# Kernel tuning notes

Measured on AMD Instinct MI355X. Metric: run time of the kernel, lower is better.

## Reference

```python
import jax, jax.numpy as jnp
import numpy as np

D_MODEL = 768
N_HEADS = 8
HEAD_DIM = D_MODEL // N_HEADS  # 96


def setup_inputs() -> dict:
    key = jax.random.key(0)
    k1, k2, k3, k4, k5 = jax.random.split(key, 5)
    B, LQ, LK = 2, 4096, 4096
    hidden_states = jax.random.normal(k1, (B, LQ, D_MODEL), dtype=jnp.float32)
    key_value_states = jax.random.normal(k2, (B, LK, D_MODEL), dtype=jnp.float32)
    # learned projection params (initialized as eye in torch, but learned; use random here)
    Wq = jax.random.normal(k3, (D_MODEL, D_MODEL), dtype=jnp.float32) * 0.02
    Wk = jax.random.normal(k4, (D_MODEL, D_MODEL), dtype=jnp.float32) * 0.02
    Wv = jax.random.normal(k5, (D_MODEL, D_MODEL), dtype=jnp.float32) * 0.02
    return {"hidden_states": hidden_states, "key_value_states": key_value_states,
            "Wq": Wq, "Wk": Wk, "Wv": Wv}


def reference(hidden_states, key_value_states, Wq, Wk, Wv):
    B, LQ, _ = hidden_states.shape
    LK = key_value_states.shape[1]
    # linear projections (no bias)
    q = hidden_states @ Wq            # [B, LQ, D]
    k = key_value_states @ Wk         # [B, LK, D]
    v = key_value_states @ Wv         # [B, LK, D]
    # split heads: [B, H, L, d]
    def shape(x, L):
        return x.reshape(B, L, N_HEADS, HEAD_DIM).transpose(0, 2, 1, 3)
    q = shape(q, LQ) / jnp.sqrt(jnp.float32(HEAD_DIM))
    k = shape(k, LK)
    v = shape(v, LK)
    scores = jnp.einsum('bhqd,bhkd->bhqk', q, k)   # [B, H, LQ, LK]
    attn = jax.nn.softmax(scores, axis=-1)
    # dropout p=0.0 -> identity
    ctx = jnp.einsum('bhqk,bhkd->bhqd', attn, v)   # [B, H, LQ, d]
    context = ctx.transpose(0, 2, 1, 3).reshape(B, LQ, D_MODEL)
    return context
```

## Files before the change

kernel.cpp:

```cpp
#include <hip/hip_runtime.h>
#include <hip/hip_bf16.h>


typedef __bf16 bf16x8 __attribute__((ext_vector_type(8)));
typedef __bf16 bf16x4 __attribute__((ext_vector_type(4)));
typedef float  f32x4  __attribute__((ext_vector_type(4)));
typedef float  f32x16 __attribute__((ext_vector_type(16)));
typedef unsigned u32x4 __attribute__((ext_vector_type(4)));

#define DM   768
#define NH   8
#define HD   96
#define SEQ  4096
#define BATCH 2
#define WELEM (DM*DM)
#define XELEM (BATCH*SEQ*DM)

#define GLDS16(gp, lp) __builtin_amdgcn_global_load_lds( \
    (const __attribute__((address_space(1))) void*)(gp), \
    (__attribute__((address_space(3))) void*)(lp), 16, 0, 0)

__global__ __launch_bounds__(256) void transpose_w3(
    const float* __restrict__ Wq, const float* __restrict__ Wk, const float* __restrict__ Wv,
    __bf16* __restrict__ Tq, __bf16* __restrict__ Tk, __bf16* __restrict__ Tv)
{
    int tid = blockIdx.x * 256 + threadIdx.x;
    int which = tid / WELEM;
    int e = tid - which * WELEM;
    int k = e / DM, n = e - k * DM;
    const float* W = (which == 0) ? Wq : (which == 1) ? Wk : Wv;
    __bf16* T      = (which == 0) ? Tq : (which == 1) ? Tk : Tv;
    T[n * DM + k] = (__bf16)W[e];
}

__global__ __launch_bounds__(256) void convert_x(
    const float* __restrict__ X0, const float* __restrict__ X1,
    __bf16* __restrict__ Y0, __bf16* __restrict__ Y1)
{
    const float* X = blockIdx.y ? X1 : X0;
    __bf16* Y      = blockIdx.y ? Y1 : Y0;
    const size_t i = ((size_t)blockIdx.x * 256 + threadIdx.x) * 8;
    float4 lo = *reinterpret_cast<const float4*>(X + i);
    float4 hi = *reinterpret_cast<const float4*>(X + i + 4);
    bf16x8 v;
    v[0]=(__bf16)lo.x; v[1]=(__bf16)lo.y; v[2]=(__bf16)lo.z; v[3]=(__bf16)lo.w;
    v[4]=(__bf16)hi.x; v[5]=(__bf16)hi.y; v[6]=(__bf16)hi.z; v[7]=(__bf16)hi.w;
    *reinterpret_cast<bf16x8*>(Y + i) = v;
}

__global__ __launch_bounds__(256, 2) void proj_gemm128(
    const __bf16* __restrict__ Xb, const __bf16* __restrict__ Wt,
    __bf16* __restrict__ Y, int mode, float scale)
{
    __shared__ __bf16 As[2][128][64];
    __shared__ __bf16 Bs[2][128][64];

    const int t = threadIdx.x;
    const int l = t & 63;
    const int w = t >> 6;
    const int ln = l & 15, g = l >> 4;
    const int wm = w >> 1, wn = w & 1;

    const int id = blockIdx.x;
    const int xcd = id & 7, c = id >> 3;
    const int m0 = (xcd * 8 + c / 6) * 128;
    const int n0 = (c % 6) * 128;

    size_t asrc[4], bsrc[4]; unsigned sdst[4];
    #pragma unroll
    for (int j = 0; j < 4; ++j) {
        const int cid = j * 256 + t;
        const int r = cid >> 3, cc = cid & 7, cs = cc ^ (r & 7);
        asrc[j] = (size_t)(m0 + r) * DM + cs * 8;
        bsrc[j] = (size_t)(n0 + r) * DM + cs * 8;
        sdst[j] = cid * 16;
    }

    f32x4 acc[4][4] = {};

    #pragma unroll
    for (int j = 0; j < 4; ++j) GLDS16(Xb + asrc[j], (char*)As + sdst[j]);
    #pragma unroll
    for (int j = 0; j < 4; ++j) GLDS16(Wt + bsrc[j], (char*)Bs + sdst[j]);
    __syncthreads();

    const int NKT = DM / 64;
    for (int kt = 0; kt < NKT; ++kt) {
        const int cur = kt & 1;
        if (kt + 1 < NKT) {
            const unsigned nb = (cur ^ 1) * 16384u;
            const size_t k0n = (size_t)(kt + 1) * 64;
            #pragma unroll
            for (int j = 0; j < 4; ++j) GLDS16(Xb + k0n + asrc[j], (char*)As + nb + sdst[j]);
            #pragma unroll
            for (int j = 0; j < 4; ++j) GLDS16(Wt + k0n + bsrc[j], (char*)Bs + nb + sdst[j]);
        }

        #pragma unroll
        for (int kk = 0; kk < 2; ++kk) {
            bf16x8 a[4], b[4];
            #pragma unroll
            for (int ms = 0; ms < 4; ++ms) {
                const int row = wm * 64 + ms * 16 + ln;
                const int slot = (kk * 4 + g) ^ (row & 7);
                a[ms] = *reinterpret_cast<const bf16x8*>(
                    (const char*)As + cur * 16384 + row * 128 + slot * 16);
            }
            #pragma unroll
            for (int ns = 0; ns < 4; ++ns) {
                const int row = wn * 64 + ns * 16 + ln;
                const int slot = (kk * 4 + g) ^ (row & 7);
                b[ns] = *reinterpret_cast<const bf16x8*>(
                    (const char*)Bs + cur * 16384 + row * 128 + slot * 16);
            }
            #pragma unroll
            for (int ms = 0; ms < 4; ++ms)
                #pragma unroll
                for (int ns = 0; ns < 4; ++ns)
                    acc[ms][ns] = __builtin_amdgcn_mfma_f32_16x16x32_bf16(
                        a[ms], b[ns], acc[ms][ns], 0, 0, 0);
        }
        __syncthreads();
    }

    #pragma unroll
    for (int ms = 0; ms < 4; ++ms) {
        #pragma unroll
        for (int ns = 0; ns < 4; ++ns) {
            const int col = n0 + wn * 64 + ns * 16 + ln;
            const int h = col / HD, d = col - h * HD;
            const int row_base = m0 + wm * 64 + ms * 16 + 4 * g;
            if (mode == 0) {
                #pragma unroll
                for (int r = 0; r < 4; ++r) {
                    const int row = row_base + r;
                    const int b_ = row >> 12, q = row & (SEQ - 1);
                    Y[(((size_t)(b_ * NH + h) * SEQ) + q) * HD + d] =
                        (__bf16)(acc[ms][ns][r] * scale);
                }
            } else {
                const int b_ = row_base >> 12, kq = row_base & (SEQ - 1);
                bf16x4 v;
                #pragma unroll
                for (int r = 0; r < 4; ++r) v[r] = (__bf16)acc[ms][ns][r];
                *reinterpret_cast<bf16x4*>(
                    &Y[((size_t)(b_ * NH + h) * HD + d) * SEQ + kq]) = v;
            }
        }
    }
}

__global__ __launch_bounds__(256, 2) void attn_kernel(
    const __bf16* __restrict__ Q, const __bf16* __restrict__ K,
    const __bf16* __restrict__ Vt, float* __restrict__ out)
{
    __shared__ __bf16 Ks[2][64][128];
    __shared__ __bf16 Vs[2][96][64];

    const int t = threadIdx.x;
    const int l = t & 63;
    const int w = t >> 6;
    const int lh = l >> 5;
    const int c31 = l & 31;

    const int swz = (blockIdx.x & 7) * 64 + (blockIdx.x >> 3);
    const int bh = swz >> 5;
    const int qb = swz & 31;
    const int b = bh >> 3, hd = bh & 7;
    const int q0 = qb * 128 + w * 32;

    const size_t base = (size_t)bh * SEQ * HD;
    const __bf16* Kg = K + base;
    const __bf16* Vg = Vt + base;

    size_t ksrc[4], vsrc[3];
    unsigned kdst[4], vdst[3];
    #pragma unroll
    for (int j = 0; j < 4; ++j) {
        const int cid = (w * 4 + j) * 64 + l;
        const int r = cid >> 4, cc = cid & 15;
        int cs = cc ^ (r & 7); if (cs >= 12) cs = 0;
        ksrc[j] = (size_t)r * HD + cs * 8;
        kdst[j] = (w * 4 + j) * 1024;
    }
    #pragma unroll
    for (int j = 0; j < 3; ++j) {
        const int cid = (w * 3 + j) * 64 + l;
        const int d = cid >> 3, cc = cid & 7;
        const int cs = cc ^ (d & 7);
        vsrc[j] = (size_t)d * SEQ + cs * 8;
        vdst[j] = (w * 3 + j) * 1024;
    }

    bf16x8 qb_[6];
    #pragma unroll
    for (int st = 0; st < 6; ++st)
        qb_[st] = *reinterpret_cast<const bf16x8*>(
            &Q[base + (size_t)(q0 + c31) * HD + st * 16 + 8 * lh]);

    f32x16 acc[3] = {};
    float m_r = -1e30f, l_r = 0.f;

    #pragma unroll
    for (int j = 0; j < 4; ++j) GLDS16(Kg + ksrc[j], (char*)Ks + kdst[j]);
    #pragma unroll
    for (int j = 0; j < 3; ++j) GLDS16(Vg + vsrc[j], (char*)Vs + vdst[j]);
    __syncthreads();

    const int NT = SEQ / 64;
    for (int kt = 0; kt < NT; ++kt) {
        const int cur = kt & 1;

        if (kt + 1 < NT) {
            const unsigned nb = (cur ^ 1);
            #pragma unroll
            for (int j = 0; j < 4; ++j)
                GLDS16(Kg + (size_t)(kt + 1) * 64 * HD + ksrc[j],
                       (char*)Ks + nb * 16384 + kdst[j]);
            #pragma unroll
            for (int j = 0; j < 3; ++j)
                GLDS16(Vg + (size_t)(kt + 1) * 64 + vsrc[j],
                       (char*)Vs + nb * 12288 + vdst[j]);
        }

        f32x16 s[2] = {};
        __builtin_amdgcn_s_setprio(1);
        #pragma unroll
        for (int ks = 0; ks < 2; ++ks) {
            const int rr = ks * 32 + c31;
            #pragma unroll
            for (int st = 0; st < 6; ++st) {
                const int slot = (2 * st + lh) ^ (rr & 7);
                bf16x8 ka = *reinterpret_cast<const bf16x8*>(
                    (const char*)Ks + cur * 16384 + rr * 256 + slot * 16);
                s[ks] = __builtin_amdgcn_mfma_f32_32x32x16_bf16(ka, qb_[st], s[ks], 0, 0, 0);
            }
        }
        __builtin_amdgcn_s_setprio(0);

        float tm = s[0][0];
        #pragma unroll
        for (int ks = 0; ks < 2; ++ks)
            #pragma unroll
            for (int r = 0; r < 16; ++r) tm = fmaxf(tm, s[ks][r]);
        {
            float ex = tm;
            asm volatile("" : "+v"(ex));
            asm("v_permlane32_swap_b32 %0, %1" : "+v"(ex), "+v"(tm));
            tm = fmaxf(tm, ex);
        }
        if (__any(tm > m_r + 8.f)) {
            const float mn = fmaxf(m_r, tm);
            const float al = __builtin_amdgcn_exp2f(m_r - mn);
            l_r *= al; m_r = mn;
            #pragma unroll
            for (int r = 0; r < 16; ++r) {
                const float ar = __shfl(al, (r & 3) + 8 * (r >> 2) + 4 * lh, 64);
                acc[0][r] *= ar; acc[1][r] *= ar; acc[2][r] *= ar;
            }
        }
        float ps = 0.f;
        #pragma unroll
        for (int ks = 0; ks < 2; ++ks)
            #pragma unroll
            for (int r = 0; r < 16; ++r) {
                const float p = __builtin_amdgcn_exp2f(s[ks][r] - m_r);
                s[ks][r] = p;
                ps += p;
            }
        {
            float ex = ps;
            asm volatile("" : "+v"(ex));
            asm("v_permlane32_swap_b32 %0, %1" : "+v"(ex), "+v"(ps));
            ps += ex;
        }
        l_r += ps;

        unsigned up[2][4][2];
        #pragma unroll
        for (int ks = 0; ks < 2; ++ks)
            #pragma unroll
            for (int qd = 0; qd < 4; ++qd)
                #pragma unroll
                for (int j = 0; j < 2; ++j)
                    asm("v_cvt_pk_bf16_f32 %0, %1, %2"
                        : "=v"(up[ks][qd][j])
                        : "v"(s[ks][4 * qd + 2 * j]), "v"(s[ks][4 * qd + 2 * j + 1]));

        #pragma unroll
        for (int kc = 0; kc < 4; ++kc) {
            const int ks = kc >> 1, cp = kc & 1;
            unsigned x0 = up[ks][2 * cp][0],     x1 = up[ks][2 * cp][1];
            unsigned y0 = up[ks][2 * cp + 1][0], y1 = up[ks][2 * cp + 1][1];
            asm("v_permlane32_swap_b32 %0, %1" : "+v"(x0), "+v"(y0));
            asm("v_permlane32_swap_b32 %0, %1" : "+v"(x1), "+v"(y1));
            u32x4 pw; pw[0] = x0; pw[1] = x1; pw[2] = y0; pw[3] = y1;
            const bf16x8 pa = __builtin_bit_cast(bf16x8, pw);
            __builtin_amdgcn_s_setprio(1);
            #pragma unroll
            for (int dt = 0; dt < 3; ++dt) {
                const int dd = dt * 32 + c31;
                const int slot = (2 * kc + lh) ^ (dd & 7);
                bf16x8 vb = *reinterpret_cast<const bf16x8*>(
                    (const char*)Vs + cur * 12288 + dd * 128 + slot * 16);
                acc[dt] = __builtin_amdgcn_mfma_f32_32x32x16_bf16(pa, vb, acc[dt], 0, 0, 0);
            }
            __builtin_amdgcn_s_setprio(0);
        }

        __syncthreads();
    }

    const float inv = 1.0f / l_r;
    #pragma unroll
    for (int r = 0; r < 16; ++r) {
        const int ql = (r & 3) + 8 * (r >> 2) + 4 * lh;
        const float ir = __shfl(inv, ql, 64);
        const int q = q0 + ql;
        float* dst = out + ((size_t)(b * SEQ + q)) * DM + hd * HD;
        #pragma unroll
        for (int dt = 0; dt < 3; ++dt)
            dst[dt * 32 + c31] = acc[dt][r] * ir;
    }
}

extern "C" void kernel_launch(void* const* d_in, const int* in_sizes, int n_in,
                              void* d_out, int out_size, void* d_ws, size_t ws_size,
                              hipStream_t stream) {
    const float* hidden = (const float*)d_in[0];
    const float* kv     = (const float*)d_in[1];
    const float* Wq     = (const float*)d_in[2];
    const float* Wk     = (const float*)d_in[3];
    const float* Wv     = (const float*)d_in[4];
    float* out = (float*)d_out;

    __bf16* Wt_q = (__bf16*)d_ws;
    __bf16* Wt_k = Wt_q + WELEM;
    __bf16* Wt_v = Wt_k + WELEM;
    __bf16* Qb   = Wt_v + WELEM;
    __bf16* Kb   = Qb + (size_t)BATCH * NH * SEQ * HD;
    __bf16* Vtb  = Kb + (size_t)BATCH * NH * SEQ * HD;

    __bf16* Xh_bf  = (__bf16*)d_out;
    __bf16* Xkv_bf = Xh_bf + XELEM;

    transpose_w3<<<3 * (WELEM / 256), 256, 0, stream>>>(Wq, Wk, Wv, Wt_q, Wt_k, Wt_v);
    convert_x<<<dim3(XELEM / 8 / 256, 2), 256, 0, stream>>>(hidden, kv, Xh_bf, Xkv_bf);

    const float qscale = 0.10206207261596575f * 1.4426950408889634f;
    proj_gemm128<<<384, 256, 0, stream>>>(Xh_bf,  Wt_q, Qb,  0, qscale);
    proj_gemm128<<<384, 256, 0, stream>>>(Xkv_bf, Wt_k, Kb,  0, 1.0f);
    proj_gemm128<<<384, 256, 0, stream>>>(Xkv_bf, Wt_v, Vtb, 1, 1.0f);

    attn_kernel<<<512, 256, 0, stream>>>(Qb, Kb, Vtb, out);
}
```

Measured before the change: 209.2 us.

## Process two 32-row query tiles per wave in attention kernel

Each wave now handles 64 query rows (two 32-row sub-tiles), so a block covers 256 queries and the grid drops from 512 to 256 blocks. Every K and V fragment read from LDS feeds two MFMAs, which halves LDS and global K/V traffic per query. The cost is more registers per thread, so launch bounds fall to one block per SIMD group. With only 256 blocks on a 256-CU device there is one wave per SIMD, leaving little latency hiding and no tail balancing.

```diff
diff --git a/kernel.cpp b/kernel.cpp
--- a/kernel.cpp
+++ b/kernel.cpp
@@ -150,7 +150,7 @@
     }
 }
 
-__global__ __launch_bounds__(256, 2) void attn_kernel(
+__global__ __launch_bounds__(256, 1) void attn_kernel(
     const __bf16* __restrict__ Q, const __bf16* __restrict__ K,
     const __bf16* __restrict__ Vt, float* __restrict__ out)
 {
@@ -163,11 +163,11 @@
     const int lh = l >> 5;
     const int c31 = l & 31;
 
-    const int swz = (blockIdx.x & 7) * 64 + (blockIdx.x >> 3);
-    const int bh = swz >> 5;
-    const int qb = swz & 31;
+    const int swz = (blockIdx.x & 7) * 32 + (blockIdx.x >> 3);
+    const int bh = swz >> 4;
+    const int qb = swz & 15;
     const int b = bh >> 3, hd = bh & 7;
-    const int q0 = qb * 128 + w * 32;
+    const int q0 = qb * 256 + w * 64;
 
     const size_t base = (size_t)bh * SEQ * HD;
     const __bf16* Kg = K + base;
@@ -192,14 +192,16 @@
         vdst[j] = (w * 3 + j) * 1024;
     }
 
-    bf16x8 qb_[6];
-    #pragma unroll
-    for (int st = 0; st < 6; ++st)
-        qb_[st] = *reinterpret_cast<const bf16x8*>(
-            &Q[base + (size_t)(q0 + c31) * HD + st * 16 + 8 * lh]);
-
-    f32x16 acc[3] = {};
-    float m_r = -1e30f, l_r = 0.f;
+    bf16x8 qf[2][6];
+    #pragma unroll
+    for (int qh = 0; qh < 2; ++qh)
+        #pragma unroll
+        for (int st = 0; st < 6; ++st)
+            qf[qh][st] = *reinterpret_cast<const bf16x8*>(
+                &Q[base + (size_t)(q0 + qh * 32 + c31) * HD + st * 16 + 8 * lh]);
+
+    f32x16 acc[2][3] = {};
+    float m_r[2] = {-1e30f, -1e30f}, l_r[2] = {0.f, 0.f};
 
     #pragma unroll
     for (int j = 0; j < 4; ++j) GLDS16(Kg + ksrc[j], (char*)Ks + kdst[j]);
@@ -223,7 +225,7 @@
                        (char*)Vs + nb * 12288 + vdst[j]);
         }
 
-        f32x16 s[2] = {};
+        f32x16 s[2][2] = {};
         __builtin_amdgcn_s_setprio(1);
         #pragma unroll
         for (int ks = 0; ks < 2; ++ks) {
@@ -233,69 +235,79 @@
                 const int slot = (2 * st + lh) ^ (rr & 7);
                 bf16x8 ka = *reinterpret_cast<const bf16x8*>(
                     (const char*)Ks + cur * 16384 + rr * 256 + slot * 16);
-                s[ks] = __builtin_amdgcn_mfma_f32_32x32x16_bf16(ka, qb_[st], s[ks], 0, 0, 0);
+                s[0][ks] = __builtin_amdgcn_mfma_f32_32x32x16_bf16(ka, qf[0][st], s[0][ks], 0, 0, 0);
+                s[1][ks] = __builtin_amdgcn_mfma_f32_32x32x16_bf16(ka, qf[1][st], s[1][ks], 0, 0, 0);
             }
         }
         __builtin_amdgcn_s_setprio(0);
 
-        float tm = s[0][0];
-        #pragma unroll
-        for (int ks = 0; ks < 2; ++ks)
-            #pragma unroll
-            for (int r = 0; r < 16; ++r) tm = fmaxf(tm, s[ks][r]);
-        {
-            float ex = tm;
+        float tm[2];
+        #pragma unroll
+        for (int qh = 0; qh < 2; ++qh) {
+            float v = s[qh][0][0];
+            #pragma unroll
+            for (int ks = 0; ks < 2; ++ks)
+                #pragma unroll
+                for (int r = 0; r < 16; ++r) v = fmaxf(v, s[qh][ks][r]);
+            float ex = v;
             asm volatile("" : "+v"(ex));
-            asm("v_permlane32_swap_b32 %0, %1" : "+v"(ex), "+v"(tm));
-            tm = fmaxf(tm, ex);
-        }
-        if (__any(tm > m_r + 8.f)) {
-            const float mn = fmaxf(m_r, tm);
-            const float al = __builtin_amdgcn_exp2f(m_r - mn);
-            l_r *= al; m_r = mn;
-            #pragma unroll
-            for (int r = 0; r < 16; ++r) {
-                const float ar = __shfl(al, (r & 3) + 8 * (r >> 2) + 4 * lh, 64);
-                acc[0][r] *= ar; acc[1][r] *= ar; acc[2][r] *= ar;
-            }
-        }
-        float ps = 0.f;
-        #pragma unroll
-        for (int ks = 0; ks < 2; ++ks)
-            #pragma unroll
-            for (int r = 0; r < 16; ++r) {
-                const float p = __builtin_amdgcn_exp2f(s[ks][r] - m_r);
-                s[ks][r] = p;
-                ps += p;
-            }
-        {
+            asm("v_permlane32_swap_b32 %0, %1" : "+v"(ex), "+v"(v));
+            tm[qh] = fmaxf(v, ex);
+        }
+        if (__any((tm[0] > m_r[0] + 8.f) || (tm[1] > m_r[1] + 8.f))) {
+            #pragma unroll
+            for (int qh = 0; qh < 2; ++qh) {
+                const float mn = fmaxf(m_r[qh], tm[qh]);
+                const float al = __builtin_amdgcn_exp2f(m_r[qh] - mn);
+                l_r[qh] *= al; m_r[qh] = mn;
+                #pragma unroll
+                for (int r = 0; r < 16; ++r) {
+                    const float ar = __shfl(al, (r & 3) + 8 * (r >> 2) + 4 * lh, 64);
+                    acc[qh][0][r] *= ar; acc[qh][1][r] *= ar; acc[qh][2][r] *= ar;
+                }
+            }
+        }
+
+        unsigned up[2][2][4][2];
+        #pragma unroll
+        for (int qh = 0; qh < 2; ++qh) {
+            float ps = 0.f;
+            #pragma unroll
+            for (int ks = 0; ks < 2; ++ks)
+                #pragma unroll
+                for (int r = 0; r < 16; ++r) {
+                    const float p = __builtin_amdgcn_exp2f(s[qh][ks][r] - m_r[qh]);
+                    s[qh][ks][r] = p;
+                    ps += p;
+                }
             float ex = ps;
             asm volatile("" : "+v"(ex));
             asm("v_permlane32_swap_b32 %0, %1" : "+v"(ex), "+v"(ps));
-            ps += ex;
-        }
-        l_r += ps;
-
-        unsigned up[2][4][2];
-        #pragma unroll
-        for (int ks = 0; ks < 2; ++ks)
-            #pragma unroll
-            for (int qd = 0; qd < 4; ++qd)
-                #pragma unroll
-                for (int j = 0; j < 2; ++j)
-                    asm("v_cvt_pk_bf16_f32 %0, %1, %2"
-                        : "=v"(up[ks][qd][j])
-                        : "v"(s[ks][4 * qd + 2 * j]), "v"(s[ks][4 * qd + 2 * j + 1]));
+            l_r[qh] += ps + ex;
+            #pragma unroll
+            for (int ks = 0; ks < 2; ++ks)
+                #pragma unroll
+                for (int qd = 0; qd < 4; ++qd)
+                    #pragma unroll
+                    for (int j = 0; j < 2; ++j)
+                        asm("v_cvt_pk_bf16_f32 %0, %1, %2"
+                            : "=v"(up[qh][ks][qd][j])
+                            : "v"(s[qh][ks][4 * qd + 2 * j]), "v"(s[qh][ks][4 * qd + 2 * j + 1]));
+        }
 
         #pragma unroll
         for (int kc = 0; kc < 4; ++kc) {
             const int ks = kc >> 1, cp = kc & 1;
-            unsigned x0 = up[ks][2 * cp][0],     x1 = up[ks][2 * cp][1];
-            unsigned y0 = up[ks][2 * cp + 1][0], y1 = up[ks][2 * cp + 1][1];
-            asm("v_permlane32_swap_b32 %0, %1" : "+v"(x0), "+v"(y0));
-            asm("v_permlane32_swap_b32 %0, %1" : "+v"(x1), "+v"(y1));
-            u32x4 pw; pw[0] = x0; pw[1] = x1; pw[2] = y0; pw[3] = y1;
-            const bf16x8 pa = __builtin_bit_cast(bf16x8, pw);
+            bf16x8 pa[2];
+            #pragma unroll
+            for (int qh = 0; qh < 2; ++qh) {
+                unsigned x0 = up[qh][ks][2 * cp][0],     x1 = up[qh][ks][2 * cp][1];
+                unsigned y0 = up[qh][ks][2 * cp + 1][0], y1 = up[qh][ks][2 * cp + 1][1];
+                asm("v_permlane32_swap_b32 %0, %1" : "+v"(x0), "+v"(y0));
+                asm("v_permlane32_swap_b32 %0, %1" : "+v"(x1), "+v"(y1));
+                u32x4 pw; pw[0] = x0; pw[1] = x1; pw[2] = y0; pw[3] = y1;
+                pa[qh] = __builtin_bit_cast(bf16x8, pw);
+            }
             __builtin_amdgcn_s_setprio(1);
             #pragma unroll
             for (int dt = 0; dt < 3; ++dt) {
@@ -303,7 +315,8 @@
                 const int slot = (2 * kc + lh) ^ (dd & 7);
                 bf16x8 vb = *reinterpret_cast<const bf16x8*>(
                     (const char*)Vs + cur * 12288 + dd * 128 + slot * 16);
-                acc[dt] = __builtin_amdgcn_mfma_f32_32x32x16_bf16(pa, vb, acc[dt], 0, 0, 0);
+                acc[0][dt] = __builtin_amdgcn_mfma_f32_32x32x16_bf16(pa[0], vb, acc[0][dt], 0, 0, 0);
+                acc[1][dt] = __builtin_amdgcn_mfma_f32_32x32x16_bf16(pa[1], vb, acc[1][dt], 0, 0, 0);
             }
             __builtin_amdgcn_s_setprio(0);
         }
@@ -311,16 +324,19 @@
         __syncthreads();
     }
 
-    const float inv = 1.0f / l_r;
-    #pragma unroll
-    for (int r = 0; r < 16; ++r) {
-        const int ql = (r & 3) + 8 * (r >> 2) + 4 * lh;
-        const float ir = __shfl(inv, ql, 64);
-        const int q = q0 + ql;
-        float* dst = out + ((size_t)(b * SEQ + q)) * DM + hd * HD;
-        #pragma unroll
-        for (int dt = 0; dt < 3; ++dt)
-            dst[dt * 32 + c31] = acc[dt][r] * ir;
+    #pragma unroll
+    for (int qh = 0; qh < 2; ++qh) {
+        const float inv = 1.0f / l_r[qh];
+        #pragma unroll
+        for (int r = 0; r < 16; ++r) {
+            const int ql = (r & 3) + 8 * (r >> 2) + 4 * lh;
+            const float ir = __shfl(inv, ql, 64);
+            const int q = q0 + qh * 32 + ql;
+            float* dst = out + ((size_t)(b * SEQ + q)) * DM + hd * HD;
+            #pragma unroll
+            for (int dt = 0; dt < 3; ++dt)
+                dst[dt * 32 + c31] = acc[qh][dt][r] * ir;
+        }
     }
 }
 
@@ -352,5 +368,5 @@
     proj_gemm128<<<384, 256, 0, stream>>>(Xkv_bf, Wt_k, Kb,  0, 1.0f);
     proj_gemm128<<<384, 256, 0, stream>>>(Xkv_bf, Wt_v, Vtb, 1, 1.0f);
 
-    attn_kernel<<<512, 256, 0, stream>>>(Qb, Kb, Vtb, out);
-}
+    attn_kernel<<<256, 256, 0, stream>>>(Qb, Kb, Vtb, out);
+}
```

After: 222.5 us. +6.4%, slower.

## Software-pipeline attention loop: overlap next QK^T with current softmax and PV

Applied to the files above, without the earlier changes.

Restructures the attention main loop so the QK^T MFMAs for the next key tile are issued before the softmax and PV of the current tile, using two score register sets. V shared memory grows to a triple buffer because V tiles now live one extra stage. The aim is to hide softmax VALU and exp latency behind matrix work. It costs more VGPRs for the second score set and more LDS, which could reduce occupancy at the two-blocks-per-CU launch bound.

```diff
diff --git a/kernel.cpp b/kernel.cpp
--- a/kernel.cpp
+++ b/kernel.cpp
@@ -155,11 +155,11 @@
     const __bf16* __restrict__ Vt, float* __restrict__ out)
 {
     __shared__ __bf16 Ks[2][64][128];
-    __shared__ __bf16 Vs[2][96][64];
-
-    const int t = threadIdx.x;
-    const int l = t & 63;
-    const int w = t >> 6;
+    __shared__ __bf16 Vs[3][96][64];
+
+    const int t_ = threadIdx.x;
+    const int l = t_ & 63;
+    const int w = t_ >> 6;
     const int lh = l >> 5;
     const int c31 = l & 31;
 
@@ -192,57 +192,47 @@
         vdst[j] = (w * 3 + j) * 1024;
     }
 
-    bf16x8 qb_[6];
+    bf16x8 qf[6];
     #pragma unroll
     for (int st = 0; st < 6; ++st)
-        qb_[st] = *reinterpret_cast<const bf16x8*>(
+        qf[st] = *reinterpret_cast<const bf16x8*>(
             &Q[base + (size_t)(q0 + c31) * HD + st * 16 + 8 * lh]);
 
     f32x16 acc[3] = {};
+    f32x16 sA0, sA1, sB0, sB1;
     float m_r = -1e30f, l_r = 0.f;
-
-    #pragma unroll
-    for (int j = 0; j < 4; ++j) GLDS16(Kg + ksrc[j], (char*)Ks + kdst[j]);
-    #pragma unroll
-    for (int j = 0; j < 3; ++j) GLDS16(Vg + vsrc[j], (char*)Vs + vdst[j]);
-    __syncthreads();
-
-    const int NT = SEQ / 64;
-    for (int kt = 0; kt < NT; ++kt) {
-        const int cur = kt & 1;
-
-        if (kt + 1 < NT) {
-            const unsigned nb = (cur ^ 1);
-            #pragma unroll
-            for (int j = 0; j < 4; ++j)
-                GLDS16(Kg + (size_t)(kt + 1) * 64 * HD + ksrc[j],
-                       (char*)Ks + nb * 16384 + kdst[j]);
-            #pragma unroll
-            for (int j = 0; j < 3; ++j)
-                GLDS16(Vg + (size_t)(kt + 1) * 64 + vsrc[j],
-                       (char*)Vs + nb * 12288 + vdst[j]);
-        }
-
-        f32x16 s[2] = {};
-        __builtin_amdgcn_s_setprio(1);
-        #pragma unroll
-        for (int ks = 0; ks < 2; ++ks) {
-            const int rr = ks * 32 + c31;
-            #pragma unroll
-            for (int st = 0; st < 6; ++st) {
-                const int slot = (2 * st + lh) ^ (rr & 7);
-                bf16x8 ka = *reinterpret_cast<const bf16x8*>(
-                    (const char*)Ks + cur * 16384 + rr * 256 + slot * 16);
-                s[ks] = __builtin_amdgcn_mfma_f32_32x32x16_bf16(ka, qb_[st], s[ks], 0, 0, 0);
-            }
-        }
-        __builtin_amdgcn_s_setprio(0);
-
-        float tm = s[0][0];
-        #pragma unroll
-        for (int ks = 0; ks < 2; ++ks)
-            #pragma unroll
-            for (int r = 0; r < 16; ++r) tm = fmaxf(tm, s[ks][r]);
+    int vcur = 0, vst = 2;
+
+    auto STAGE = [&](int tile, int kp, int vbuf) {
+        const size_t ko = (size_t)tile * 64 * HD;
+        #pragma unroll
+        for (int j = 0; j < 4; ++j)
+            GLDS16(Kg + ko + ksrc[j], (char*)Ks + kp * 16384 + kdst[j]);
+        const size_t vo = (size_t)tile * 64;
+        #pragma unroll
+        for (int j = 0; j < 3; ++j)
+            GLDS16(Vg + vo + vsrc[j], (char*)Vs + vbuf * 12288 + vdst[j]);
+    };
+
+    auto QKT = [&](int pbuf, f32x16& S0, f32x16& S1) {
+        S0 = (f32x16){}; S1 = (f32x16){};
+        #pragma unroll
+        for (int st = 0; st < 6; ++st) {
+            const int slot = (2 * st + lh) ^ (c31 & 7);
+            bf16x8 ka0 = *reinterpret_cast<const bf16x8*>(
+                (const char*)Ks + pbuf * 16384 + c31 * 256 + slot * 16);
+            bf16x8 ka1 = *reinterpret_cast<const bf16x8*>(
+                (const char*)Ks + pbuf * 16384 + (32 + c31) * 256 + slot * 16);
+            S0 = __builtin_amdgcn_mfma_f32_32x32x16_bf16(ka0, qf[st], S0, 0, 0, 0);
+            S1 = __builtin_amdgcn_mfma_f32_32x32x16_bf16(ka1, qf[st], S1, 0, 0, 0);
+        }
+    };
+
+    auto SMPV = [&](f32x16& S0, f32x16& S1) {
+        float t0 = S0[0], t1 = S1[0];
+        #pragma unroll
+        for (int r = 1; r < 16; ++r) { t0 = fmaxf(t0, S0[r]); t1 = fmaxf(t1, S1[r]); }
+        float tm = fmaxf(t0, t1);
         {
             float ex = tm;
             asm volatile("" : "+v"(ex));
@@ -259,34 +249,33 @@
                 acc[0][r] *= ar; acc[1][r] *= ar; acc[2][r] *= ar;
             }
         }
-        float ps = 0.f;
-        #pragma unroll
-        for (int ks = 0; ks < 2; ++ks)
-            #pragma unroll
-            for (int r = 0; r < 16; ++r) {
-                const float p = __builtin_amdgcn_exp2f(s[ks][r] - m_r);
-                s[ks][r] = p;
-                ps += p;
-            }
+        float p0 = 0.f, p1 = 0.f;
+        #pragma unroll
+        for (int r = 0; r < 16; ++r) {
+            const float e0 = __builtin_amdgcn_exp2f(S0[r] - m_r);
+            const float e1 = __builtin_amdgcn_exp2f(S1[r] - m_r);
+            S0[r] = e0; S1[r] = e1; p0 += e0; p1 += e1;
+        }
+        float ps = p0 + p1;
         {
             float ex = ps;
             asm volatile("" : "+v"(ex));
             asm("v_permlane32_swap_b32 %0, %1" : "+v"(ex), "+v"(ps));
-            ps += ex;
-        }
-        l_r += ps;
-
+            l_r += ps + ex;
+        }
         unsigned up[2][4][2];
         #pragma unroll
-        for (int ks = 0; ks < 2; ++ks)
-            #pragma unroll
-            for (int qd = 0; qd < 4; ++qd)
-                #pragma unroll
-                for (int j = 0; j < 2; ++j)
-                    asm("v_cvt_pk_bf16_f32 %0, %1, %2"
-                        : "=v"(up[ks][qd][j])
-                        : "v"(s[ks][4 * qd + 2 * j]), "v"(s[ks][4 * qd + 2 * j + 1]));
-
+        for (int qd = 0; qd < 4; ++qd)
+            #pragma unroll
+            for (int j = 0; j < 2; ++j) {
+                asm("v_cvt_pk_bf16_f32 %0, %1, %2"
+                    : "=v"(up[0][qd][j])
+                    : "v"(S0[4 * qd + 2 * j]), "v"(S0[4 * qd + 2 * j + 1]));
+                asm("v_cvt_pk_bf16_f32 %0, %1, %2"
+                    : "=v"(up[1][qd][j])
+                    : "v"(S1[4 * qd + 2 * j]), "v"(S1[4 * qd + 2 * j + 1]));
+            }
+        const unsigned vbo = vcur * 12288;
         #pragma unroll
         for (int kc = 0; kc < 4; ++kc) {
             const int ks = kc >> 1, cp = kc & 1;
@@ -302,13 +291,31 @@
                 const int dd = dt * 32 + c31;
                 const int slot = (2 * kc + lh) ^ (dd & 7);
                 bf16x8 vb = *reinterpret_cast<const bf16x8*>(
-                    (const char*)Vs + cur * 12288 + dd * 128 + slot * 16);
+                    (const char*)Vs + vbo + dd * 128 + slot * 16);
                 acc[dt] = __builtin_amdgcn_mfma_f32_32x32x16_bf16(pa, vb, acc[dt], 0, 0, 0);
             }
             __builtin_amdgcn_s_setprio(0);
         }
-
+        vcur = (vcur == 2) ? 0 : vcur + 1;
+        vst  = (vst  == 2) ? 0 : vst  + 1;
+    };
+
+    STAGE(0, 0, 0);
+    __syncthreads();
+    STAGE(1, 1, 1);
+    QKT(0, sA0, sA1);
+
+    const int NT = SEQ / 64;
+    for (int u2 = 0; u2 < NT / 2; ++u2) {
+        const int u = 2 * u2;
         __syncthreads();
+        if (u + 2 < NT) STAGE(u + 2, 0, vst);
+        QKT(1, sB0, sB1);
+        SMPV(sA0, sA1);
+        __syncthreads();
+        if (u + 3 < NT) STAGE(u + 3, 1, vst);
+        if (u + 2 < NT) QKT(0, sA0, sA1);
+        SMPV(sB0, sB1);
     }
 
     const float inv = 1.0f / l_r;
@@ -338,8 +345,8 @@
     __bf16* Wt_k = Wt_q + WELEM;
     __bf16* Wt_v = Wt_k + WELEM;
     __bf16* Qb   = Wt_v + WELEM;
-    __bf16* Kb   = Qb + (size_t)BATCH * NH * SEQ * HD;
-    __bf16* Vtb  = Kb + (size_t)BATCH * NH * SEQ * HD;
+    __bf16* Kb   = Qb + XELEM;
+    __bf16* Vtb  = Kb + XELEM;
 
     __bf16* Xh_bf  = (__bf16*)d_out;
     __bf16* Xkv_bf = Xh_bf + XELEM;
```

Measured after the change: 204.1 us. 2.4% less time.
